# Kernel optimization log

Measured on AMD Instinct MI355X. Metric: run time of the kernel, lower is better.

Reference implementation:

```python
import jax, jax.numpy as jnp
import numpy as np

L, B, E, H, NL = 512, 8, 1024, 16, 2
HD = E // H
DFF = 4 * E
EPS = 1e-5


def setup_inputs() -> dict:
    key = jax.random.key(0)
    ks = jax.random.split(key, 8)
    s = 0.02
    return {
        "src": jax.random.normal(ks[0], (L, B, E), jnp.float32),
        "position_embed": jax.random.normal(ks[1], (L, L, HD), jnp.float32) * s,
        "type_embed": jax.random.normal(ks[2], (L, L, HD), jnp.float32) * s,
        "Wi": jax.random.normal(ks[3], (NL, 3 * E, E), jnp.float32) * s,
        "bi": jnp.zeros((NL, 3 * E), jnp.float32),
        "Wo": jax.random.normal(ks[4], (NL, E, E), jnp.float32) * s,
        "bo": jnp.zeros((NL, E), jnp.float32),
        "W1": jax.random.normal(ks[5], (NL, DFF, E), jnp.float32) * s,
        "b1": jnp.zeros((NL, DFF), jnp.float32),
        "W2": jax.random.normal(ks[6], (NL, E, DFF), jnp.float32) * s,
        "b2": jnp.zeros((NL, E), jnp.float32),
        "g1": jnp.ones((NL, E), jnp.float32),
        "be1": jnp.zeros((NL, E), jnp.float32),
        "g2": jnp.ones((NL, E), jnp.float32),
        "be2": jnp.zeros((NL, E), jnp.float32),
    }


def _ln(x, g, b):
    m = jnp.mean(x, -1, keepdims=True)
    v = jnp.mean((x - m) ** 2, -1, keepdims=True)
    return (x - m) * jax.lax.rsqrt(v + EPS) * g + b


def _attn(src, pos, typ, Wi, bi, Wo, bo):
    # src: [L, B, E]
    p = src @ Wi.T + bi                      # [L, B, 3E]
    q, k, v = jnp.split(p, 3, axis=-1)
    q = q * (HD ** -0.5)
    # -> [B, H, L, HD]
    def hsplit(t):
        return t.reshape(L, B, H, HD).transpose(1, 2, 0, 3)
    q, k, v = hsplit(q), hsplit(k), hsplit(v)
    # scores = q k^T + type_embed@q + q@pos^T  (Shaw relative attention)
    scores = jnp.einsum('bhld,bhsd->bhls', q, k)
    scores = scores + jnp.einsum('bhld,lsd->bhls', q, pos)      # position term
    scores = scores + jnp.einsum('lsd,bhld->bhls', typ, q)      # type term
    w = jax.nn.softmax(scores, axis=-1)                          # [B, H, L, S]
    # output = w v + w@pos + typ^T@w
    out = jnp.einsum('bhls,bhsd->bhld', w, v)
    out = out + jnp.einsum('bhls,lsd->bhld', w, pos)
    out = out + jnp.einsum('bhls,lsd->bhld', w, typ)
    out = out.transpose(2, 0, 1, 3).reshape(L, B, E)            # [L, B, E]
    return out @ Wo.T + bo


def _layer(src, pos, typ, Wi, bi, Wo, bo, W1, b1, W2, b2, g1, be1, g2, be2):
    src2 = _attn(src, pos, typ, Wi, bi, Wo, bo)
    src = _ln(src + src2, g1, be1)
    h = jax.nn.gelu(src @ W1.T + b1, approximate=False)
    src2 = h @ W2.T + b2
    return _ln(src + src2, g2, be2)


def reference(src, position_embed, type_embed, Wi, bi, Wo, bo, W1, b1, W2, b2,
              g1, be1, g2, be2):
    out = src
    for i in range(NL):
        out = _layer(out, position_embed, type_embed,
                     Wi[i], bi[i], Wo[i], bo[i], W1[i], b1[i], W2[i], b2[i],
                     g1[i], be1[i], g2[i], be2[i])
    return out
```

## Files before the change

kernel.cpp:

```cpp
#include <hip/hip_runtime.h>
#include <hip/hip_bf16.h>
#include <math.h>


typedef __hip_bfloat16 bf16;
typedef short short8 __attribute__((ext_vector_type(8)));
typedef float f32x4 __attribute__((ext_vector_type(4)));

typedef __attribute__((address_space(1))) const void gvoid;
typedef __attribute__((address_space(3))) void lvoid;

constexpr int Lc = 512;
constexpr int Bc = 8;
constexpr int Ec = 1024;
constexpr int Hc = 16;
constexpr int HDc = 64;
constexpr int NLc = 2;
constexpr int DFFc = 4096;
constexpr int LB = Lc * Bc;
constexpr int BHc = Bc * Hc;
constexpr float EPSc = 1e-5f;

__device__ inline unsigned short f2bfu(float f) {
  union { __hip_bfloat16 h; unsigned short u; } cv;
  cv.h = __float2bfloat16(f);
  return cv.u;
}

template <bool ACC, bool GELU, bool OBF>
__global__ __launch_bounds__(256) void gemm_bt128d(
    int M, int N, int K,
    const bf16* __restrict__ A, int lda, long long sAz,
    const bf16* __restrict__ Bm, int ldb, long long sBz,
    void* __restrict__ Cv, int ldc, long long sCz,
    const float* __restrict__ bias) {
  __shared__ __align__(16) bf16 As[2 * 128 * 64];
  __shared__ __align__(16) bf16 Bs[2 * 128 * 64];
  const int tid = threadIdx.x;
  const int w = tid >> 6, lane = tid & 63, quad = lane >> 4, lr = lane & 15;
  const int wr = w >> 1, wc = w & 1;
  const int m0 = blockIdx.x * 128, n0 = blockIdx.y * 128;
  const long long z = blockIdx.z;
  A += z * sAz;
  Bm += z * sBz;
  float* Cf = (float*)Cv;
  bf16* Cb = (bf16*)Cv;

  f32x4 acc[4][4];
#pragma unroll
  for (int i = 0; i < 4; i++)
#pragma unroll
    for (int j = 0; j < 4; j++) acc[i][j] = {0.f, 0.f, 0.f, 0.f};

  const int rA = lane >> 3;
  const int cA = ((lane & 7) ^ (lane >> 3)) * 8;

  auto STAGE = [&](int buf, int kt) {
    const int k0 = kt << 6;
#pragma unroll
    for (int t = 0; t < 4; ++t) {
      const int chunk = w * 4 + t;
      const int row = chunk * 8 + rA;
      __builtin_amdgcn_global_load_lds(
          (gvoid*)(A + (long long)(m0 + row) * lda + k0 + cA),
          (lvoid*)(As + buf * 8192 + chunk * 512), 16, 0, 0);
      __builtin_amdgcn_global_load_lds(
          (gvoid*)(Bm + (long long)(n0 + row) * ldb + k0 + cA),
          (lvoid*)(Bs + buf * 8192 + chunk * 512), 16, 0, 0);
    }
  };

  auto COMPUTE = [&](int buf) {
    const char* Ab = (const char*)(As + buf * 8192);
    const char* Bb = (const char*)(Bs + buf * 8192);
#pragma unroll
    for (int ks = 0; ks < 64; ks += 32) {
      const int swzc = (ks * 2 + quad * 16) ^ ((lr & 7) << 4);
      short8 a[4], b[4];
#pragma unroll
      for (int i = 0; i < 4; i++)
        a[i] = *(const short8*)(Ab + (wr * 64 + i * 16 + lr) * 128 + swzc);
#pragma unroll
      for (int j = 0; j < 4; j++)
        b[j] = *(const short8*)(Bb + (wc * 64 + j * 16 + lr) * 128 + swzc);
#pragma unroll
      for (int i = 0; i < 4; i++)
#pragma unroll
        for (int j = 0; j < 4; j++)
          acc[i][j] = __builtin_amdgcn_mfma_f32_16x16x32_bf16(a[i], b[j], acc[i][j], 0, 0, 0);
    }
  };

  const int nt = K >> 6;
  STAGE(0, 0);
  __syncthreads();

  int cur = 0;
  for (int t = 0; t < nt - 1; ++t) {
    STAGE(cur ^ 1, t + 1);
    __builtin_amdgcn_sched_barrier(0);
    COMPUTE(cur);
    __syncthreads();
    cur ^= 1;
  }
  COMPUTE(cur);

#pragma unroll
  for (int i = 0; i < 4; i++) {
#pragma unroll
    for (int j = 0; j < 4; j++) {
      int col = n0 + wc * 64 + j * 16 + lr;
      float bv = bias ? bias[col] : 0.f;
#pragma unroll
      for (int r = 0; r < 4; r++) {
        int row = m0 + wr * 64 + i * 16 + quad * 4 + r;
        long long off = z * sCz + (long long)row * ldc + col;
        float v = acc[i][j][r] + bv;
        if (ACC) v += Cf[off];
        if (GELU) v = 0.5f * v * (1.f + erff(v * 0.70710678118654752f));
        if (OBF)
          Cb[off] = __float2bfloat16(v);
        else
          Cf[off] = v;
      }
    }
  }
}

template <bool ACC, bool GELU, bool OBF>
__global__ __launch_bounds__(256) void gemm_bt(
    int M, int N, int K,
    const bf16* __restrict__ A, int lda, long long sAz,
    const bf16* __restrict__ Bm, int ldb, long long sBz,
    void* __restrict__ Cv, int ldc, long long sCz,
    const float* __restrict__ bias) {
  __shared__ __align__(16) bf16 As[128 * 72];
  __shared__ __align__(16) bf16 Bs[64 * 72];
  const int tid = threadIdx.x;
  const int w = tid >> 6, lane = tid & 63, quad = lane >> 4, lr = lane & 15;
  const int m0 = blockIdx.x * 128, n0 = blockIdx.y * 64;
  const long long z = blockIdx.z;
  A += z * sAz;
  Bm += z * sBz;
  float* Cf = (float*)Cv;
  bf16* Cb = (bf16*)Cv;

  f32x4 acc[2][4];
#pragma unroll
  for (int i = 0; i < 2; i++)
#pragma unroll
    for (int j = 0; j < 4; j++) acc[i][j] = {0.f, 0.f, 0.f, 0.f};

  for (int k0 = 0; k0 < K; k0 += 64) {
#pragma unroll
    for (int i = 0; i < 8; i++) {
      int slot = tid + i * 256;
      int r = slot >> 4, c4 = (slot & 15) << 2;
      const bf16* srcp = A + (long long)(m0 + r) * lda + k0 + c4;
      *(ushort4*)&As[r * 72 + c4] = *(const ushort4*)srcp;
    }
#pragma unroll
    for (int i = 0; i < 4; i++) {
      int slot = tid + i * 256;
      int r = slot >> 4, c4 = (slot & 15) << 2;
      const bf16* srcp = Bm + (long long)(n0 + r) * ldb + k0 + c4;
      *(ushort4*)&Bs[r * 72 + c4] = *(const ushort4*)srcp;
    }
    __syncthreads();
#pragma unroll
    for (int ks = 0; ks < 64; ks += 32) {
      short8 a[2], b[4];
#pragma unroll
      for (int i = 0; i < 2; i++)
        a[i] = *(const short8*)&As[(w * 32 + i * 16 + lr) * 72 + ks + quad * 8];
#pragma unroll
      for (int j = 0; j < 4; j++)
        b[j] = *(const short8*)&Bs[(j * 16 + lr) * 72 + ks + quad * 8];
#pragma unroll
      for (int i = 0; i < 2; i++)
#pragma unroll
        for (int j = 0; j < 4; j++)
          acc[i][j] = __builtin_amdgcn_mfma_f32_16x16x32_bf16(a[i], b[j], acc[i][j], 0, 0, 0);
    }
    __syncthreads();
  }

#pragma unroll
  for (int i = 0; i < 2; i++) {
#pragma unroll
    for (int j = 0; j < 4; j++) {
      int col = n0 + j * 16 + lr;
      float bv = bias ? bias[col] : 0.f;
#pragma unroll
      for (int r = 0; r < 4; r++) {
        int row = m0 + w * 32 + i * 16 + quad * 4 + r;
        long long off = z * sCz + (long long)row * ldc + col;
        float v = acc[i][j][r] + bv;
        if (ACC) v += Cf[off];
        if (GELU) v = 0.5f * v * (1.f + erff(v * 0.70710678118654752f));
        if (OBF)
          Cb[off] = __float2bfloat16(v);
        else
          Cf[off] = v;
      }
    }
  }
}

__global__ void cvt_bf16(const float* __restrict__ in, bf16* __restrict__ out, long long n) {
  long long i = (long long)blockIdx.x * 256 + threadIdx.x;
  if (i < n) out[i] = __float2bfloat16(in[i]);
}

__global__ void init_x(const float* __restrict__ src, float* __restrict__ x, bf16* __restrict__ xb) {
  long long i = (long long)blockIdx.x * 256 + threadIdx.x;
  float v = src[i];
  x[i] = v;
  xb[i] = __float2bfloat16(v);
}

__global__ void prep_R(const float* __restrict__ pos, const float* __restrict__ typ,
                       bf16* __restrict__ Rb, bf16* __restrict__ Rt) {
  __shared__ __align__(16) float Ls[64 * 68];
  int l = blockIdx.y, s0 = blockIdx.x * 64;
  int tid = threadIdx.x;
#pragma unroll
  for (int i = 0; i < 4; i++) {
    int slot = tid + i * 256;
    int r = slot >> 4, c = (slot & 15) << 2;
    long long off = (((long long)l) * Lc + s0 + r) * HDc + c;
    float4 a = *(const float4*)&pos[off];
    float4 b = *(const float4*)&typ[off];
    float4 s = {a.x + b.x, a.y + b.y, a.z + b.z, a.w + b.w};
    *(float4*)&Ls[r * 68 + c] = s;
    ushort4 o = {f2bfu(s.x), f2bfu(s.y), f2bfu(s.z), f2bfu(s.w)};
    *(ushort4*)&Rb[off] = o;
  }
  __syncthreads();
#pragma unroll
  for (int i = 0; i < 4; i++) {
    int slot = tid + i * 256;
    int d = slot >> 4, s4 = (slot & 15) << 2;
    ushort4 o = {f2bfu(Ls[(s4 + 0) * 68 + d]), f2bfu(Ls[(s4 + 1) * 68 + d]),
                 f2bfu(Ls[(s4 + 2) * 68 + d]), f2bfu(Ls[(s4 + 3) * 68 + d])};
    *(ushort4*)&Rt[(((long long)l) * HDc + d) * Lc + s0 + s4] = o;
  }
}

__global__ void split_qk(const float* __restrict__ P, bf16* __restrict__ q, bf16* __restrict__ k) {
  long long idx = (long long)blockIdx.x * 256 + threadIdx.x;
  int col = idx & (Ec - 1);
  long long row = idx >> 10;
  int l = (int)(row >> 3), b = (int)(row & 7);
  int h = col >> 6, d = col & 63;
  long long dst = (((long long)(b * Hc + h)) * Lc + l) * HDc + d;
  q[dst] = __float2bfloat16(P[row * 3072 + col] * 0.125f);
  k[dst] = __float2bfloat16(P[row * 3072 + Ec + col]);
}

__global__ void transpose_v(const float* __restrict__ P, bf16* __restrict__ vt) {
  __shared__ __align__(16) float Ls[64 * 68];
  int bh = blockIdx.y, b = bh >> 4, h = bh & 15;
  int l0 = blockIdx.x * 64;
  int tid = threadIdx.x;
#pragma unroll
  for (int i = 0; i < 4; i++) {
    int slot = tid + i * 256;
    int r = slot >> 4, c = (slot & 15) << 2;
    float4 v = *(const float4*)&P[((long long)(l0 + r) * Bc + b) * 3072 + 2 * Ec + h * 64 + c];
    *(float4*)&Ls[r * 68 + c] = v;
  }
  __syncthreads();
#pragma unroll
  for (int i = 0; i < 4; i++) {
    int slot = tid + i * 256;
    int d = slot >> 4, s4 = (slot & 15) << 2;
    ushort4 o = {f2bfu(Ls[(s4 + 0) * 68 + d]), f2bfu(Ls[(s4 + 1) * 68 + d]),
                 f2bfu(Ls[(s4 + 2) * 68 + d]), f2bfu(Ls[(s4 + 3) * 68 + d])};
    *(ushort4*)&vt[(((long long)(b * Hc + h)) * HDc + d) * Lc + l0 + s4] = o;
  }
}

__global__ __launch_bounds__(256) void softmax_rows(const float* S, bf16* P) {
  int w = threadIdx.x >> 6, lane = threadIdx.x & 63;
  long long row = (long long)blockIdx.x * 4 + w;
  const float* sr = S + row * 512;
  float4 v0 = *(const float4*)(sr + lane * 4);
  float4 v1 = *(const float4*)(sr + 256 + lane * 4);
  float mx = fmaxf(fmaxf(fmaxf(v0.x, v0.y), fmaxf(v0.z, v0.w)),
                   fmaxf(fmaxf(v1.x, v1.y), fmaxf(v1.z, v1.w)));
#pragma unroll
  for (int o = 32; o; o >>= 1) mx = fmaxf(mx, __shfl_xor(mx, o, 64));
  float e[8];
  e[0] = __expf(v0.x - mx); e[1] = __expf(v0.y - mx);
  e[2] = __expf(v0.z - mx); e[3] = __expf(v0.w - mx);
  e[4] = __expf(v1.x - mx); e[5] = __expf(v1.y - mx);
  e[6] = __expf(v1.z - mx); e[7] = __expf(v1.w - mx);
  float sum = e[0] + e[1] + e[2] + e[3] + e[4] + e[5] + e[6] + e[7];
#pragma unroll
  for (int o = 32; o; o >>= 1) sum += __shfl_xor(sum, o, 64);
  float inv = 1.f / sum;
  ushort4 o0 = {f2bfu(e[0] * inv), f2bfu(e[1] * inv), f2bfu(e[2] * inv), f2bfu(e[3] * inv)};
  ushort4 o1 = {f2bfu(e[4] * inv), f2bfu(e[5] * inv), f2bfu(e[6] * inv), f2bfu(e[7] * inv)};
  *(ushort4*)(P + row * 1024 + lane * 4) = o0;
  *(ushort4*)(P + row * 1024 + 256 + lane * 4) = o1;
}

__global__ void merge_ao(const float* __restrict__ ao2, bf16* __restrict__ aob) {
  long long i = (long long)blockIdx.x * 256 + threadIdx.x;
  int d = (int)(i & 63);
  long long t = i >> 6;
  int l = (int)(t & (Lc - 1));
  long long bh = t >> 9;
  int b = (int)(bh >> 4), h = (int)(bh & 15);
  aob[((long long)(l * Bc + b)) * Ec + h * 64 + d] = __float2bfloat16(ao2[i]);
}

__global__ __launch_bounds__(256) void add_ln(const float* __restrict__ X, const float* __restrict__ Cin,
                                              const float* __restrict__ g, const float* __restrict__ be,
                                              float* __restrict__ outF, bf16* __restrict__ outB) {
  __shared__ float s_sum[4], s_sq[4];
  long long row = blockIdx.x;
  int tid = threadIdx.x;
  float4 xv = *(const float4*)&X[row * Ec + tid * 4];
  float4 cv = *(const float4*)&Cin[row * Ec + tid * 4];
  float v[4] = {xv.x + cv.x, xv.y + cv.y, xv.z + cv.z, xv.w + cv.w};
  float sm = v[0] + v[1] + v[2] + v[3];
  float sq = v[0] * v[0] + v[1] * v[1] + v[2] * v[2] + v[3] * v[3];
#pragma unroll
  for (int o = 32; o; o >>= 1) {
    sm += __shfl_xor(sm, o, 64);
    sq += __shfl_xor(sq, o, 64);
  }
  int w = tid >> 6, lane = tid & 63;
  if (lane == 0) {
    s_sum[w] = sm;
    s_sq[w] = sq;
  }
  __syncthreads();
  sm = s_sum[0] + s_sum[1] + s_sum[2] + s_sum[3];
  sq = s_sq[0] + s_sq[1] + s_sq[2] + s_sq[3];
  float mean = sm * (1.f / Ec);
  float var = sq * (1.f / Ec) - mean * mean;
  float rs = rsqrtf(var + EPSc);
#pragma unroll
  for (int e = 0; e < 4; e++) {
    int n = tid * 4 + e;
    float o = (v[e] - mean) * rs * g[n] + be[n];
    outF[row * Ec + n] = o;
    outB[row * Ec + n] = __float2bfloat16(o);
  }
}

static constexpr size_t WS_NEED = 327155712;

struct GlobalWs {
  void* p = nullptr;
  GlobalWs() {
    if (hipMalloc(&p, WS_NEED) != hipSuccess) p = nullptr;
  }
};
static GlobalWs g_ws;

extern "C" void kernel_launch(void* const* d_in, const int* in_sizes, int n_in,
                              void* d_out, int out_size, void* d_ws, size_t ws_size,
                              hipStream_t stream) {
  const float* src = (const float*)d_in[0];
  const float* pos = (const float*)d_in[1];
  const float* typ = (const float*)d_in[2];
  const float* Wi = (const float*)d_in[3];
  const float* bi = (const float*)d_in[4];
  const float* Wo = (const float*)d_in[5];
  const float* bo = (const float*)d_in[6];
  const float* W1 = (const float*)d_in[7];
  const float* b1 = (const float*)d_in[8];
  const float* W2 = (const float*)d_in[9];
  const float* b2 = (const float*)d_in[10];
  const float* g1 = (const float*)d_in[11];
  const float* be1 = (const float*)d_in[12];
  const float* g2 = (const float*)d_in[13];
  const float* be2 = (const float*)d_in[14];
  float* out = (float*)d_out;
  (void)in_sizes; (void)n_in; (void)out_size;

  char* wp = (ws_size >= WS_NEED) ? (char*)d_ws : (char*)g_ws.p;
  if (!wp) wp = (char*)d_ws;
  auto alloc = [&](size_t bytes) {
    char* r = wp;
    wp += (bytes + 255) & ~(size_t)255;
    return r;
  };

  char* U = alloc((size_t)BHc * Lc * Lc * 4);
  float* P = (float*)U;
  float* scores = (float*)U;
  bf16* probs = (bf16*)U;
  bf16* hb = (bf16*)U;

  float* x = (float*)alloc((size_t)LB * Ec * 4);
  bf16* xb = (bf16*)alloc((size_t)LB * Ec * 2);
  bf16* q = (bf16*)alloc((size_t)BHc * Lc * HDc * 2);
  bf16* k = (bf16*)alloc((size_t)BHc * Lc * HDc * 2);
  bf16* vt = (bf16*)alloc((size_t)BHc * HDc * Lc * 2);
  float* ao2 = (float*)alloc((size_t)BHc * Lc * HDc * 4);
  float* c1 = ao2;
  bf16* aob = (bf16*)alloc((size_t)LB * Ec * 2);
  bf16* Rb = (bf16*)alloc((size_t)Lc * Lc * HDc * 2);
  bf16* Rt = (bf16*)alloc((size_t)Lc * HDc * Lc * 2);
  bf16* wib = (bf16*)alloc((size_t)NLc * 3 * Ec * Ec * 2);
  bf16* wob = (bf16*)alloc((size_t)NLc * Ec * Ec * 2);
  bf16* w1b = (bf16*)alloc((size_t)NLc * DFFc * Ec * 2);
  bf16* w2b = (bf16*)alloc((size_t)NLc * Ec * DFFc * 2);

  {
    long long n;
    n = (long long)NLc * 3 * Ec * Ec;
    cvt_bf16<<<(int)((n + 255) / 256), 256, 0, stream>>>(Wi, wib, n);
    n = (long long)NLc * Ec * Ec;
    cvt_bf16<<<(int)((n + 255) / 256), 256, 0, stream>>>(Wo, wob, n);
    n = (long long)NLc * DFFc * Ec;
    cvt_bf16<<<(int)((n + 255) / 256), 256, 0, stream>>>(W1, w1b, n);
    n = (long long)NLc * Ec * DFFc;
    cvt_bf16<<<(int)((n + 255) / 256), 256, 0, stream>>>(W2, w2b, n);
  }
  prep_R<<<dim3(Lc / 64, Lc), 256, 0, stream>>>(pos, typ, Rb, Rt);
  init_x<<<LB * Ec / 256, 256, 0, stream>>>(src, x, xb);

  for (int i = 0; i < NLc; i++) {
    const bf16* Wi_b = wib + (size_t)i * 3 * Ec * Ec;
    const bf16* Wo_b = wob + (size_t)i * Ec * Ec;
    const bf16* W1_b = w1b + (size_t)i * DFFc * Ec;
    const bf16* W2_b = w2b + (size_t)i * Ec * DFFc;

    gemm_bt128d<false, false, false><<<dim3(LB / 128, 3 * Ec / 128, 1), 256, 0, stream>>>(
        LB, 3 * Ec, Ec, xb, Ec, 0, Wi_b, Ec, 0, P, 3 * Ec, 0, bi + (size_t)i * 3 * Ec);
    split_qk<<<LB * Ec / 256, 256, 0, stream>>>(P, q, k);
    transpose_v<<<dim3(Lc / 64, BHc), 256, 0, stream>>>(P, vt);

    gemm_bt<false, false, false><<<dim3(Lc / 128, Lc / 64, BHc), 256, 0, stream>>>(
        Lc, Lc, HDc, q, HDc, (long long)Lc * HDc, k, HDc, (long long)Lc * HDc,
        scores, Lc, (long long)Lc * Lc, nullptr);
    gemm_bt<true, false, false><<<dim3(1, Lc / 64, Lc), 256, 0, stream>>>(
        BHc, Lc, HDc, q, Lc * HDc, (long long)HDc, Rb, HDc, (long long)Lc * HDc,
        scores, Lc * Lc, (long long)Lc, nullptr);

    softmax_rows<<<BHc * Lc / 4, 256, 0, stream>>>(scores, probs);

    gemm_bt<false, false, false><<<dim3(Lc / 128, 1, BHc), 256, 0, stream>>>(
        Lc, HDc, Lc, probs, 1024, (long long)Lc * 1024, vt, Lc, (long long)HDc * Lc,
        ao2, HDc, (long long)Lc * HDc, nullptr);
    gemm_bt<true, false, false><<<dim3(1, 1, Lc), 256, 0, stream>>>(
        BHc, HDc, Lc, probs, Lc * 1024, (long long)1024, Rt, Lc, (long long)HDc * Lc,
        ao2, Lc * HDc, (long long)HDc, nullptr);

    merge_ao<<<BHc * Lc * HDc / 256, 256, 0, stream>>>(ao2, aob);

    gemm_bt128d<false, false, false><<<dim3(LB / 128, Ec / 128, 1), 256, 0, stream>>>(
        LB, Ec, Ec, aob, Ec, 0, Wo_b, Ec, 0, c1, Ec, 0, bo + (size_t)i * Ec);
    add_ln<<<LB, 256, 0, stream>>>(x, c1, g1 + (size_t)i * Ec, be1 + (size_t)i * Ec, x, xb);

    gemm_bt128d<false, true, true><<<dim3(LB / 128, DFFc / 128, 1), 256, 0, stream>>>(
        LB, DFFc, Ec, xb, Ec, 0, W1_b, Ec, 0, hb, DFFc, 0, b1 + (size_t)i * DFFc);
    gemm_bt128d<false, false, false><<<dim3(LB / 128, Ec / 128, 1), 256, 0, stream>>>(
        LB, Ec, DFFc, hb, DFFc, 0, W2_b, DFFc, 0, c1, Ec, 0, b2 + (size_t)i * Ec);

    float* outF = (i == NLc - 1) ? out : x;
    add_ln<<<LB, 256, 0, stream>>>(x, c1, g2 + (size_t)i * Ec, be2 + (size_t)i * Ec, outF, xb);
  }
}
```

Measured before the change: 1.214 ms.

## Split-K the Wo/W2 GEMMs with LN-fused reduction and prefetch LDS fragments

The Wo and W2 projection GEMMs are split along K into two slices launched as a z-dimension of 2, each writing a separate fp32 partial buffer. A new add_ln4 kernel sums the residual, the bias and both partials before layernorm. This doubles the workgroup count for these 256-tile GEMMs to fill more CUs, at the cost of extra partial-buffer traffic. The 64-wide GEMM main loop is also restructured: LDS fragments for the whole tile are loaded before issuing the next global->LDS stage, MFMAs run at raised priority, and __syncthreads is replaced by an explicit vmcnt wait plus s_barrier.

```diff
diff --git a/kernel.cpp b/kernel.cpp
--- a/kernel.cpp
+++ b/kernel.cpp
@@ -70,40 +70,59 @@
     }
   };
 
-  auto COMPUTE = [&](int buf) {
+  auto LOAD = [&](int buf, short8 (&a)[2][4], short8 (&b)[2][4]) {
     const char* Ab = (const char*)(As + buf * 8192);
     const char* Bb = (const char*)(Bs + buf * 8192);
 #pragma unroll
-    for (int ks = 0; ks < 64; ks += 32) {
-      const int swzc = (ks * 2 + quad * 16) ^ ((lr & 7) << 4);
-      short8 a[4], b[4];
+    for (int ks2 = 0; ks2 < 2; ks2++) {
+      const int swzc = (ks2 * 64 + quad * 16) ^ ((lr & 7) << 4);
 #pragma unroll
       for (int i = 0; i < 4; i++)
-        a[i] = *(const short8*)(Ab + (wr * 64 + i * 16 + lr) * 128 + swzc);
+        a[ks2][i] = *(const short8*)(Ab + (wr * 64 + i * 16 + lr) * 128 + swzc);
 #pragma unroll
       for (int j = 0; j < 4; j++)
-        b[j] = *(const short8*)(Bb + (wc * 64 + j * 16 + lr) * 128 + swzc);
+        b[ks2][j] = *(const short8*)(Bb + (wc * 64 + j * 16 + lr) * 128 + swzc);
+    }
+  };
+
+  auto MMA = [&](short8 (&a)[2][4], short8 (&b)[2][4]) {
+#pragma unroll
+    for (int ks2 = 0; ks2 < 2; ks2++)
 #pragma unroll
       for (int i = 0; i < 4; i++)
 #pragma unroll
         for (int j = 0; j < 4; j++)
-          acc[i][j] = __builtin_amdgcn_mfma_f32_16x16x32_bf16(a[i], b[j], acc[i][j], 0, 0, 0);
-    }
+          acc[i][j] = __builtin_amdgcn_mfma_f32_16x16x32_bf16(a[ks2][i], b[ks2][j], acc[i][j], 0, 0, 0);
   };
 
   const int nt = K >> 6;
   STAGE(0, 0);
-  __syncthreads();
+  asm volatile("s_waitcnt vmcnt(0)" ::: "memory");
+  __builtin_amdgcn_sched_barrier(0);
+  __builtin_amdgcn_s_barrier();
+  __builtin_amdgcn_sched_barrier(0);
 
   int cur = 0;
   for (int t = 0; t < nt - 1; ++t) {
+    short8 a[2][4], b[2][4];
+    LOAD(cur, a, b);
+    __builtin_amdgcn_sched_barrier(0);
     STAGE(cur ^ 1, t + 1);
     __builtin_amdgcn_sched_barrier(0);
-    COMPUTE(cur);
-    __syncthreads();
+    __builtin_amdgcn_s_setprio(1);
+    MMA(a, b);
+    __builtin_amdgcn_s_setprio(0);
+    asm volatile("s_waitcnt vmcnt(0)" ::: "memory");
+    __builtin_amdgcn_sched_barrier(0);
+    __builtin_amdgcn_s_barrier();
+    __builtin_amdgcn_sched_barrier(0);
     cur ^= 1;
   }
-  COMPUTE(cur);
+  {
+    short8 a[2][4], b[2][4];
+    LOAD(cur, a, b);
+    MMA(a, b);
+  }
 
 #pragma unroll
   for (int i = 0; i < 4; i++) {
@@ -316,15 +335,21 @@
   aob[((long long)(l * Bc + b)) * Ec + h * 64 + d] = __float2bfloat16(ao2[i]);
 }
 
-__global__ __launch_bounds__(256) void add_ln(const float* __restrict__ X, const float* __restrict__ Cin,
-                                              const float* __restrict__ g, const float* __restrict__ be,
-                                              float* __restrict__ outF, bf16* __restrict__ outB) {
+__global__ __launch_bounds__(256) void add_ln4(
+    const float* __restrict__ X, const float* __restrict__ Pp, long long pstride, int ns,
+    const float* __restrict__ bias,
+    const float* __restrict__ g, const float* __restrict__ be,
+    float* __restrict__ outF, bf16* __restrict__ outB) {
   __shared__ float s_sum[4], s_sq[4];
   long long row = blockIdx.x;
   int tid = threadIdx.x;
   float4 xv = *(const float4*)&X[row * Ec + tid * 4];
-  float4 cv = *(const float4*)&Cin[row * Ec + tid * 4];
-  float v[4] = {xv.x + cv.x, xv.y + cv.y, xv.z + cv.z, xv.w + cv.w};
+  float4 bv = *(const float4*)&bias[tid * 4];
+  float v[4] = {xv.x + bv.x, xv.y + bv.y, xv.z + bv.z, xv.w + bv.w};
+  for (int s = 0; s < ns; ++s) {
+    float4 pv = *(const float4*)&Pp[s * pstride + row * Ec + tid * 4];
+    v[0] += pv.x; v[1] += pv.y; v[2] += pv.z; v[3] += pv.w;
+  }
   float sm = v[0] + v[1] + v[2] + v[3];
   float sq = v[0] * v[0] + v[1] * v[1] + v[2] * v[2] + v[3] * v[3];
 #pragma unroll
@@ -396,6 +421,8 @@
   float* scores = (float*)U;
   bf16* probs = (bf16*)U;
   bf16* hb = (bf16*)U;
+  float* part = (float*)(U + (size_t)34 * 1024 * 1024);
+  const long long PSTRIDE = (long long)LB * Ec;
 
   float* x = (float*)alloc((size_t)LB * Ec * 4);
   bf16* xb = (bf16*)alloc((size_t)LB * Ec * 2);
@@ -403,7 +430,6 @@
   bf16* k = (bf16*)alloc((size_t)BHc * Lc * HDc * 2);
   bf16* vt = (bf16*)alloc((size_t)BHc * HDc * Lc * 2);
   float* ao2 = (float*)alloc((size_t)BHc * Lc * HDc * 4);
-  float* c1 = ao2;
   bf16* aob = (bf16*)alloc((size_t)LB * Ec * 2);
   bf16* Rb = (bf16*)alloc((size_t)Lc * Lc * HDc * 2);
   bf16* Rt = (bf16*)alloc((size_t)Lc * HDc * Lc * 2);
@@ -455,16 +481,20 @@
 
     merge_ao<<<BHc * Lc * HDc / 256, 256, 0, stream>>>(ao2, aob);
 
-    gemm_bt128d<false, false, false><<<dim3(LB / 128, Ec / 128, 1), 256, 0, stream>>>(
-        LB, Ec, Ec, aob, Ec, 0, Wo_b, Ec, 0, c1, Ec, 0, bo + (size_t)i * Ec);
-    add_ln<<<LB, 256, 0, stream>>>(x, c1, g1 + (size_t)i * Ec, be1 + (size_t)i * Ec, x, xb);
+    gemm_bt128d<false, false, false><<<dim3(LB / 128, Ec / 128, 2), 256, 0, stream>>>(
+        LB, Ec, Ec / 2, aob, Ec, (long long)(Ec / 2), Wo_b, Ec, (long long)(Ec / 2),
+        part, Ec, PSTRIDE, nullptr);
+    add_ln4<<<LB, 256, 0, stream>>>(x, part, PSTRIDE, 2, bo + (size_t)i * Ec,
+                                    g1 + (size_t)i * Ec, be1 + (size_t)i * Ec, x, xb);
 
     gemm_bt128d<false, true, true><<<dim3(LB / 128, DFFc / 128, 1), 256, 0, stream>>>(
         LB, DFFc, Ec, xb, Ec, 0, W1_b, Ec, 0, hb, DFFc, 0, b1 + (size_t)i * DFFc);
-    gemm_bt128d<false, false, false><<<dim3(LB / 128, Ec / 128, 1), 256, 0, stream>>>(
-        LB, Ec, DFFc, hb, DFFc, 0, W2_b, DFFc, 0, c1, Ec, 0, b2 + (size_t)i * Ec);
+    gemm_bt128d<false, false, false><<<dim3(LB / 128, Ec / 128, 2), 256, 0, stream>>>(
+        LB, Ec, DFFc / 2, hb, DFFc, (long long)(DFFc / 2), W2_b, DFFc, (long long)(DFFc / 2),
+        part, Ec, PSTRIDE, nullptr);
 
     float* outF = (i == NLc - 1) ? out : x;
-    add_ln<<<LB, 256, 0, stream>>>(x, c1, g2 + (size_t)i * Ec, be2 + (size_t)i * Ec, outF, xb);
-  }
-}
+    add_ln4<<<LB, 256, 0, stream>>>(x, part, PSTRIDE, 2, b2 + (size_t)i * Ec,
+                                    g2 + (size_t)i * Ec, be2 + (size_t)i * Ec, outF, xb);
+  }
+}
```

Measured after the change: 1.097 ms. 9.6% less time.
